# Optimization experiments

Measured on AMD Instinct MI355X. Metric: run time of the kernel, lower is better.

Reference implementation:

```python
import jax, jax.numpy as jnp
import numpy as np

B, S, H, D = 1, 2048, 16, 128
CAUSAL = True


def setup_inputs() -> dict:
    key = jax.random.key(0)
    kq, kk, kv = jax.random.split(key, 3)
    query = jax.random.normal(kq, (B, S, H, D), dtype=jnp.float32)
    k_ = jax.random.normal(kk, (B, S, H, D), dtype=jnp.float32)
    v_ = jax.random.normal(kv, (B, S, H, D), dtype=jnp.float32)
    return {"query": query, "key": k_, "value": v_}


def reference(query, key, value):
    # Single-device equivalent of LongContextAttention:
    # Ulysses all-to-all and ring pass are identity on one rank; the math is
    # standard scaled-dot-product attention with flash-attn's default scale
    # softmax_scale = 1/sqrt(head_dim) and causal masking.
    d = query.shape[-1]
    scale = 1.0 / jnp.sqrt(jnp.asarray(d, dtype=query.dtype))
    # [B,S,H,D] x [B,T,H,D] -> [B,H,S,T]
    scores = jnp.einsum("bshd,bthd->bhst", query, key) * scale
    if CAUSAL:
        s, t = scores.shape[-2], scores.shape[-1]
        mask = jnp.tril(jnp.ones((s, t), dtype=bool))
        scores = jnp.where(mask, scores, jnp.finfo(scores.dtype).min)
    probs = jax.nn.softmax(scores, axis=-1)
    out = jnp.einsum("bhst,bthd->bshd", probs, value)
    return out
```

## Files before the change

kernel.cpp:

```cpp
#include <hip/hip_runtime.h>
#include <hip/hip_bf16.h>
#include <math.h>

#define SS 2048
#define HH 16
#define DD 128
#define HD (HH*DD)
#define QB 128
#define KVB 64
#define CHUNK 7
#define NJ 46

typedef __attribute__((ext_vector_type(8))) short bf16x8;
typedef __attribute__((ext_vector_type(16))) float f32x16;

__device__ __forceinline__ ushort f2bf(float f) {
  __hip_bfloat16 h = __float2bfloat16(f);
  return __builtin_bit_cast(ushort, h);
}
__device__ __forceinline__ uint pk2(float a, float b) {
  return ((uint)f2bf(b) << 16) | (uint)f2bf(a);
}
__device__ __forceinline__ float bf2f(ushort u) {
  uint x = ((uint)u) << 16;
  return __builtin_bit_cast(float, x);
}
__device__ __forceinline__ void gld16(const void* g, void* l) {
  __builtin_amdgcn_global_load_lds(
      (const __attribute__((address_space(1))) void*)g,
      (__attribute__((address_space(3))) void*)l, 16, 0, 0);
}

__constant__ const int JBc[17] = {0,1,2,3,5,7,9,11,14,17,20,24,28,32,36,41,46};

__global__ __launch_bounds__(256, 4)
void prep_kv(const float* __restrict__ K, const float* __restrict__ V,
             ushort* __restrict__ Kbf, ushort* __restrict__ VTg) {
  __shared__ ushort Vlds[64][136];
  const int tid = threadIdx.x;
  const int h  = blockIdx.x & 15;
  const int tc = blockIdx.x >> 4;
  const int t0 = tc * 64;

  #pragma unroll
  for (int j = 0; j < 2; ++j) {
    int li = tid + j * 256;
    int t  = li >> 3;
    int c  = (li & 7) << 4;
    const float* src = K + ((size_t)(t0 + t) * HH + h) * DD + c;
    ushort tmp[16];
    #pragma unroll
    for (int q = 0; q < 4; ++q) {
      float4 x = *(const float4*)(src + 4 * q);
      tmp[4*q+0] = f2bf(x.x); tmp[4*q+1] = f2bf(x.y);
      tmp[4*q+2] = f2bf(x.z); tmp[4*q+3] = f2bf(x.w);
    }
    ushort* dst = Kbf + ((size_t)h * SS + t0 + t) * DD + c;
    *(uint4*)dst       = *(uint4*)&tmp[0];
    *(uint4*)(dst + 8) = *(uint4*)&tmp[8];
  }

  #pragma unroll
  for (int j = 0; j < 2; ++j) {
    int li = tid + j * 256;
    int t  = li >> 3;
    int c  = (li & 7) << 4;
    const float* src = V + ((size_t)(t0 + t) * HH + h) * DD + c;
    #pragma unroll
    for (int q = 0; q < 4; ++q) {
      float4 x = *(const float4*)(src + 4 * q);
      ushort4 w; w.x = f2bf(x.x); w.y = f2bf(x.y); w.z = f2bf(x.z); w.w = f2bf(x.w);
      *(ushort4*)&Vlds[t][c + 4 * q] = w;
    }
  }
  __syncthreads();

  #pragma unroll
  for (int j = 0; j < 2; ++j) {
    int li  = tid + j * 256;
    int d   = li >> 2;
    int t16 = (li & 3) << 4;
    ushort tmp[16];
    #pragma unroll
    for (int k = 0; k < 16; ++k) tmp[k] = Vlds[t16 + k][d];
    ushort* dst = VTg + (((size_t)h * 32 + tc) * DD + d) * 64 + t16;
    *(uint4*)dst       = *(uint4*)&tmp[0];
    *(uint4*)(dst + 8) = *(uint4*)&tmp[8];
  }
}

__global__ __launch_bounds__(256, 2)
void attn_fwd(const float* __restrict__ Q, const ushort* __restrict__ Kbf,
              const ushort* __restrict__ VTg, float* __restrict__ O,
              ushort* __restrict__ PO, float* __restrict__ PM,
              float* __restrict__ PL) {
  __shared__ alignas(16) ushort Klds[2][KVB * DD];
  __shared__ alignas(16) ushort VTlds[2][DD * KVB];

  const int tid  = threadIdx.x;
  const int lane = tid & 63;
  const int wid  = tid >> 6;
  const int q32  = lane & 31;
  const int hi   = lane >> 5;
  const int kxk  = (q32 & 15) << 4;
  const int kxv  = ((q32 & 7) << 4) ^ ((q32 & 8) << 1);

  int koff[4], voff[4];
  #pragma unroll
  for (int k2 = 0; k2 < 4; ++k2) {
    int b = wid * 4096 + k2 * 1024 + 16 * lane;
    int krow = b >> 8;
    koff[k2] = b ^ ((krow & 15) << 4);
    int d = b >> 7;
    voff[k2] = b ^ (((d & 7) << 4) ^ ((d & 8) << 1));
  }

  const int bx = blockIdx.x;
  const int h  = bx & 15;
  const int j  = bx >> 4;
  int qt = 0, c = 0;
  #pragma unroll
  for (int q2 = 15; q2 >= 0; --q2) {
    if (j >= JBc[q2]) { qt = q2; c = j - JBc[q2]; break; }
  }
  const int nt  = 2 * qt + 2;
  const int lo  = CHUNK * c;
  const int hiT = min(lo + CHUNK, nt);
  const int nc  = JBc[qt + 1] - JBc[qt];

  const float SCALE = 1.44269504088896f / sqrtf((float)DD);
  const char* KG = (const char*)Kbf + (size_t)h * SS * DD * 2;
  const char* VG = (const char*)VTg + (size_t)h * 32 * 16384;

  auto issueK = [&](int t0, int buf) {
    const char* gt = KG + (size_t)t0 * 256;
    char* lb = (char*)&Klds[buf][0] + wid * 4096;
    #pragma unroll
    for (int k2 = 0; k2 < 4; ++k2)
      gld16(gt + koff[k2], lb + k2 * 1024);
  };
  auto issueV = [&](int tc, int buf) {
    const char* gt = VG + (size_t)tc * 16384;
    char* lb = (char*)&VTlds[buf][0] + wid * 4096;
    #pragma unroll
    for (int k2 = 0; k2 < 4; ++k2)
      gld16(gt + voff[k2], lb + k2 * 1024);
  };

  const int qw = qt * QB + 32 * wid;
  const int qg = qw + q32;

  bf16x8 qf[8];
  {
    const float* qr = Q + ((size_t)qg * HH + h) * DD;
    #pragma unroll
    for (int ks = 0; ks < 8; ++ks) {
      float4 x = *(const float4*)&qr[16 * ks + 8 * hi];
      float4 y = *(const float4*)&qr[16 * ks + 8 * hi + 4];
      uint4 u;
      u.x = pk2(x.x * SCALE, x.y * SCALE);
      u.y = pk2(x.z * SCALE, x.w * SCALE);
      u.z = pk2(y.x * SCALE, y.y * SCALE);
      u.w = pk2(y.z * SCALE, y.w * SCALE);
      qf[ks] = __builtin_bit_cast(bf16x8, u);
    }
  }

  f32x16 acc[4];
  #pragma unroll
  for (int dt = 0; dt < 4; ++dt)
    #pragma unroll
    for (int e = 0; e < 16; ++e) acc[dt][e] = 0.f;
  float m = -1e30f, l = 0.f;

  issueK(lo * KVB, 0);
  issueV(lo, 0);
  int cur = 0;

  for (int itile = lo; itile < hiT; ++itile) {
    __syncthreads();
    const bool more = (itile + 1 < hiT);
    if (more) {
      issueK((itile + 1) * KVB, cur ^ 1);
      issueV(itile + 1, cur ^ 1);
    }

    const int t0 = itile * KVB;
    const char* Kc = (const char*)&Klds[cur][0];
    const char* Vc = (const char*)&VTlds[cur][0];

    f32x16 s0, s1;
    #pragma unroll
    for (int e = 0; e < 16; ++e) { s0[e] = 0.f; s1[e] = 0.f; }
    __builtin_amdgcn_s_setprio(1);
    #pragma unroll
    for (int ks = 0; ks < 8; ++ks) {
      bf16x8 a0 = *(const bf16x8*)(Kc + ((q32 * 256 + 32 * ks + 16 * hi) ^ kxk));
      s0 = __builtin_amdgcn_mfma_f32_32x32x16_bf16(a0, qf[ks], s0, 0, 0, 0);
      bf16x8 a1 = *(const bf16x8*)(Kc + (((q32 + 32) * 256 + 32 * ks + 16 * hi) ^ kxk));
      s1 = __builtin_amdgcn_mfma_f32_32x32x16_bf16(a1, qf[ks], s1, 0, 0, 0);
    }
    __builtin_amdgcn_s_setprio(0);

    if (t0 + KVB - 1 > qw) {
      #pragma unroll
      for (int e = 0; e < 16; ++e) {
        int tloc = (e & 3) + 8 * (e >> 2) + 4 * hi;
        if (t0 + tloc > qg)      s0[e] = -INFINITY;
        if (t0 + 32 + tloc > qg) s1[e] = -INFINITY;
      }
    }

    float tmx[8];
    #pragma unroll
    for (int e = 0; e < 8; ++e)
      tmx[e] = fmaxf(fmaxf(s0[e], s0[e + 8]), fmaxf(s1[e], s1[e + 8]));
    #pragma unroll
    for (int st = 4; st >= 1; st >>= 1)
      #pragma unroll
      for (int e = 0; e < st; ++e) tmx[e] = fmaxf(tmx[e], tmx[e + st]);
    float mr = fmaxf(tmx[0], __shfl_xor(tmx[0], 32));

    if (!__all(mr <= m + 8.0f)) {
      float mn = fmaxf(m, mr);
      float corr = exp2f(m - mn);
      m = mn;
      l *= corr;
      #pragma unroll
      for (int dt = 0; dt < 4; ++dt)
        #pragma unroll
        for (int e = 0; e < 16; ++e) acc[dt][e] *= corr;
    }

    float ts[8];
    #pragma unroll
    for (int e = 0; e < 8; ++e) ts[e] = 0.f;
    #pragma unroll
    for (int e = 0; e < 16; ++e) {
      float p0 = exp2f(s0[e] - m); s0[e] = p0;
      float p1 = exp2f(s1[e] - m); s1[e] = p1;
      ts[e & 7] += p0 + p1;
    }
    #pragma unroll
    for (int st = 4; st >= 1; st >>= 1)
      #pragma unroll
      for (int e = 0; e < st; ++e) ts[e] += ts[e + st];
    float ps = ts[0] + __shfl_xor(ts[0], 32);
    l += ps;

    uint4 paf[4];
    #pragma unroll
    for (int tk = 0; tk < 4; ++tk) {
      float p0,p1,p2,p3,p4,p5,p6,p7;
      if (tk == 0) { p0=s0[0];p1=s0[1];p2=s0[2];p3=s0[3];p4=s0[4];p5=s0[5];p6=s0[6];p7=s0[7]; }
      else if (tk == 1) { p0=s0[8];p1=s0[9];p2=s0[10];p3=s0[11];p4=s0[12];p5=s0[13];p6=s0[14];p7=s0[15]; }
      else if (tk == 2) { p0=s1[0];p1=s1[1];p2=s1[2];p3=s1[3];p4=s1[4];p5=s1[5];p6=s1[6];p7=s1[7]; }
      else { p0=s1[8];p1=s1[9];p2=s1[10];p3=s1[11];p4=s1[12];p5=s1[13];p6=s1[14];p7=s1[15]; }
      uint A0 = pk2(p0, p1), A1 = pk2(p2, p3);
      uint B0 = pk2(p4, p5), B1 = pk2(p6, p7);
      uint x0 = hi ? A0 : B0, x1 = hi ? A1 : B1;
      uint r0 = (uint)__shfl_xor((int)x0, 32);
      uint r1 = (uint)__shfl_xor((int)x1, 32);
      paf[tk].x = hi ? r0 : A0;
      paf[tk].y = hi ? r1 : A1;
      paf[tk].z = hi ? B0 : r0;
      paf[tk].w = hi ? B1 : r1;
    }

    __builtin_amdgcn_s_setprio(1);
    #pragma unroll
    for (int tk = 0; tk < 4; ++tk) {
      bf16x8 pb = __builtin_bit_cast(bf16x8, paf[tk]);
      #pragma unroll
      for (int dt = 0; dt < 4; ++dt) {
        bf16x8 va = *(const bf16x8*)(Vc +
                      (((dt * 32 + q32) * 128 + 32 * tk + 16 * hi) ^ kxv));
        acc[dt] = __builtin_amdgcn_mfma_f32_32x32x16_bf16(va, pb, acc[dt], 0, 0, 0);
      }
    }
    __builtin_amdgcn_s_setprio(0);

    cur ^= 1;
  }

  const int row = 32 * wid + q32;
  if (nc == 1) {
    float invl = 1.0f / l;
    float* op = O + ((size_t)(qt * QB + row) * HH + h) * DD;
    #pragma unroll
    for (int dt = 0; dt < 4; ++dt) {
      #pragma unroll
      for (int rq = 0; rq < 4; ++rq) {
        int d = 32 * dt + 8 * rq + 4 * hi;
        float4 x = make_float4(acc[dt][4 * rq + 0] * invl, acc[dt][4 * rq + 1] * invl,
                               acc[dt][4 * rq + 2] * invl, acc[dt][4 * rq + 3] * invl);
        *(float4*)&op[d] = x;
      }
    }
  } else {
    ushort* po = PO + (size_t)bx * (QB * DD);
    #pragma unroll
    for (int dt = 0; dt < 4; ++dt) {
      #pragma unroll
      for (int rq = 0; rq < 4; ++rq) {
        int d = 32 * dt + 8 * rq + 4 * hi;
        uint2 w;
        w.x = pk2(acc[dt][4 * rq + 0], acc[dt][4 * rq + 1]);
        w.y = pk2(acc[dt][4 * rq + 2], acc[dt][4 * rq + 3]);
        *(uint2*)&po[row * DD + d] = w;
      }
    }
    if (hi == 0) {
      PM[(size_t)bx * QB + row] = m;
      PL[(size_t)bx * QB + row] = l;
    }
  }
}

__global__ __launch_bounds__(256, 2)
void attn_merge(const ushort* __restrict__ PO, const float* __restrict__ PM,
                const float* __restrict__ PL, float* __restrict__ O) {
  const int bx  = blockIdx.x;
  const int h   = bx & 15;
  const int qt  = 3 + (bx >> 4);
  const int tid = threadIdx.x;
  const int r   = tid >> 1;
  const int dh  = (tid & 1) * 64;

  const int base = JBc[qt];
  const int nc   = JBc[qt + 1] - JBc[qt];

  float M = -1e30f;
  for (int cc = 0; cc < nc; ++cc) {
    int slot = (base + cc) * 16 + h;
    M = fmaxf(M, PM[(size_t)slot * QB + r]);
  }
  float L = 0.f;
  float o[64];
  #pragma unroll
  for (int k2 = 0; k2 < 64; ++k2) o[k2] = 0.f;
  for (int cc = 0; cc < nc; ++cc) {
    int slot = (base + cc) * 16 + h;
    float w = exp2f(PM[(size_t)slot * QB + r] - M);
    L += PL[(size_t)slot * QB + r] * w;
    const ushort* src = PO + (size_t)slot * (QB * DD) + r * DD + dh;
    #pragma unroll
    for (int k4 = 0; k4 < 16; ++k4) {
      ushort4 u = *(const ushort4*)&src[4 * k4];
      o[4*k4+0] += bf2f(u.x) * w;
      o[4*k4+1] += bf2f(u.y) * w;
      o[4*k4+2] += bf2f(u.z) * w;
      o[4*k4+3] += bf2f(u.w) * w;
    }
  }
  float inv = 1.0f / L;
  float* op = O + ((size_t)(qt * QB + r) * HH + h) * DD + dh;
  #pragma unroll
  for (int k4 = 0; k4 < 16; ++k4) {
    float4 x = make_float4(o[4*k4]*inv, o[4*k4+1]*inv, o[4*k4+2]*inv, o[4*k4+3]*inv);
    *(float4*)&op[4 * k4] = x;
  }
}

extern "C" void kernel_launch(void* const* d_in, const int* in_sizes, int n_in,
                              void* d_out, int out_size, void* d_ws, size_t ws_size,
                              hipStream_t stream) {
  const float* Q = (const float*)d_in[0];
  const float* K = (const float*)d_in[1];
  const float* V = (const float*)d_in[2];
  float* O = (float*)d_out;

  const size_t kv_elems = (size_t)HH * SS * DD;
  ushort* Kbf = (ushort*)d_ws;
  ushort* VTg = Kbf + kv_elems;
  ushort* PO  = VTg + kv_elems;
  float*  PM  = (float*)(PO + (size_t)(NJ * 16) * QB * DD);
  float*  PL  = PM + (size_t)(NJ * 16) * QB;

  prep_kv<<<dim3(HH * (SS / 64)), 256, 0, stream>>>(K, V, Kbf, VTg);
  attn_fwd<<<dim3(NJ * 16), 256, 0, stream>>>(Q, Kbf, VTg, O, PO, PM, PL);
  attn_merge<<<dim3(13 * 16), 256, 0, stream>>>(PO, PM, PL, O);
}
```

Measured before the change: 78.66 us.

## Convert K to bf16 inside attention kernel and rebalance split-KV work chunks

Removes the K conversion from the prep kernel. The attention kernel now loads fp32 K into registers, packs it to bf16 and stores it into swizzled LDS mid-iteration, so the load overlaps with compute. The split-KV partition changes from fixed 7-tile chunks to an even split per query tile (38 work items), and blocks are launched heaviest-first by reversing the index. This trades a K prep pass and its global round trip for more register pressure and doubled fp32 K reads per block.

Measured after the change: 77.46 us. Within noise of the previous version (-1.5%).

```diff
diff --git a/kernel.cpp b/kernel.cpp
--- a/kernel.cpp
+++ b/kernel.cpp
@@ -8,8 +8,7 @@
 #define HD (HH*DD)
 #define QB 128
 #define KVB 64
-#define CHUNK 7
-#define NJ 46
+#define NJ 38
 
 typedef __attribute__((ext_vector_type(8))) short bf16x8;
 typedef __attribute__((ext_vector_type(16))) float f32x16;
@@ -31,11 +30,10 @@
       (__attribute__((address_space(3))) void*)l, 16, 0, 0);
 }
 
-__constant__ const int JBc[17] = {0,1,2,3,5,7,9,11,14,17,20,24,28,32,36,41,46};
+__constant__ const int JB2c[17] = {0,1,2,3,4,6,8,10,12,14,17,20,23,26,30,34,38};
 
 __global__ __launch_bounds__(256, 4)
-void prep_kv(const float* __restrict__ K, const float* __restrict__ V,
-             ushort* __restrict__ Kbf, ushort* __restrict__ VTg) {
+void prep_v(const float* __restrict__ V, ushort* __restrict__ VTg) {
   __shared__ ushort Vlds[64][136];
   const int tid = threadIdx.x;
   const int h  = blockIdx.x & 15;
@@ -47,24 +45,6 @@
     int li = tid + j * 256;
     int t  = li >> 3;
     int c  = (li & 7) << 4;
-    const float* src = K + ((size_t)(t0 + t) * HH + h) * DD + c;
-    ushort tmp[16];
-    #pragma unroll
-    for (int q = 0; q < 4; ++q) {
-      float4 x = *(const float4*)(src + 4 * q);
-      tmp[4*q+0] = f2bf(x.x); tmp[4*q+1] = f2bf(x.y);
-      tmp[4*q+2] = f2bf(x.z); tmp[4*q+3] = f2bf(x.w);
-    }
-    ushort* dst = Kbf + ((size_t)h * SS + t0 + t) * DD + c;
-    *(uint4*)dst       = *(uint4*)&tmp[0];
-    *(uint4*)(dst + 8) = *(uint4*)&tmp[8];
-  }
-
-  #pragma unroll
-  for (int j = 0; j < 2; ++j) {
-    int li = tid + j * 256;
-    int t  = li >> 3;
-    int c  = (li & 7) << 4;
     const float* src = V + ((size_t)(t0 + t) * HH + h) * DD + c;
     #pragma unroll
     for (int q = 0; q < 4; ++q) {
@@ -90,7 +70,7 @@
 }
 
 __global__ __launch_bounds__(256, 2)
-void attn_fwd(const float* __restrict__ Q, const ushort* __restrict__ Kbf,
+void attn_fwd(const float* __restrict__ Q, const float* __restrict__ K,
               const ushort* __restrict__ VTg, float* __restrict__ O,
               ushort* __restrict__ PO, float* __restrict__ PM,
               float* __restrict__ PL) {
@@ -105,39 +85,50 @@
   const int kxk  = (q32 & 15) << 4;
   const int kxv  = ((q32 & 7) << 4) ^ ((q32 & 8) << 1);
 
-  int koff[4], voff[4];
+  int voff[4];
   #pragma unroll
   for (int k2 = 0; k2 < 4; ++k2) {
     int b = wid * 4096 + k2 * 1024 + 16 * lane;
-    int krow = b >> 8;
-    koff[k2] = b ^ ((krow & 15) << 4);
     int d = b >> 7;
     voff[k2] = b ^ (((d & 7) << 4) ^ ((d & 8) << 1));
   }
 
   const int bx = blockIdx.x;
   const int h  = bx & 15;
-  const int j  = bx >> 4;
+  const int jrev = (NJ - 1) - (bx >> 4);
   int qt = 0, c = 0;
   #pragma unroll
   for (int q2 = 15; q2 >= 0; --q2) {
-    if (j >= JBc[q2]) { qt = q2; c = j - JBc[q2]; break; }
+    if (jrev >= JB2c[q2]) { qt = q2; c = jrev - JB2c[q2]; break; }
   }
   const int nt  = 2 * qt + 2;
-  const int lo  = CHUNK * c;
-  const int hiT = min(lo + CHUNK, nt);
-  const int nc  = JBc[qt + 1] - JBc[qt];
+  const int nc  = JB2c[qt + 1] - JB2c[qt];
+  const int lo  = (c * nt) / nc;
+  const int hiT = ((c + 1) * nt) / nc;
 
   const float SCALE = 1.44269504088896f / sqrtf((float)DD);
-  const char* KG = (const char*)Kbf + (size_t)h * SS * DD * 2;
-  const char* VG = (const char*)VTg + (size_t)h * 32 * 16384;
-
-  auto issueK = [&](int t0, int buf) {
-    const char* gt = KG + (size_t)t0 * 256;
-    char* lb = (char*)&Klds[buf][0] + wid * 4096;
-    #pragma unroll
-    for (int k2 = 0; k2 < 4; ++k2)
-      gld16(gt + koff[k2], lb + k2 * 1024);
+  const float* Kb = K + (size_t)h * DD;
+  const char*  VG = (const char*)VTg + (size_t)h * 32 * 16384;
+
+  uint4 kreg[4];
+  auto loadK = [&](int t0) {
+    #pragma unroll
+    for (int it = 0; it < 4; ++it) {
+      int e = tid + it * 256;
+      int row = e >> 4, col = (e & 15) * 8;
+      const float* src = &Kb[(size_t)(t0 + row) * HD + col];
+      float4 a = *(const float4*)src;
+      float4 b = *(const float4*)(src + 4);
+      kreg[it].x = pk2(a.x, a.y); kreg[it].y = pk2(a.z, a.w);
+      kreg[it].z = pk2(b.x, b.y); kreg[it].w = pk2(b.z, b.w);
+    }
+  };
+  auto stageK = [&](int buf) {
+    #pragma unroll
+    for (int it = 0; it < 4; ++it) {
+      int e = tid + it * 256;
+      *(uint4*)((char*)&Klds[buf][0] + ((e * 16) ^ (e & 0xF0))) = kreg[it];
+    }
   };
   auto issueV = [&](int tc, int buf) {
     const char* gt = VG + (size_t)tc * 16384;
@@ -173,16 +164,17 @@
     for (int e = 0; e < 16; ++e) acc[dt][e] = 0.f;
   float m = -1e30f, l = 0.f;
 
-  issueK(lo * KVB, 0);
+  loadK(lo * KVB);
   issueV(lo, 0);
+  stageK(0);
   int cur = 0;
 
   for (int itile = lo; itile < hiT; ++itile) {
     __syncthreads();
     const bool more = (itile + 1 < hiT);
     if (more) {
-      issueK((itile + 1) * KVB, cur ^ 1);
       issueV(itile + 1, cur ^ 1);
+      loadK((itile + 1) * KVB);
     }
 
     const int t0 = itile * KVB;
@@ -267,6 +259,8 @@
       paf[tk].w = hi ? B1 : r1;
     }
 
+    if (more) stageK(cur ^ 1);
+
     __builtin_amdgcn_s_setprio(1);
     #pragma unroll
     for (int tk = 0; tk < 4; ++tk) {
@@ -322,17 +316,16 @@
                 const float* __restrict__ PL, float* __restrict__ O) {
   const int bx  = blockIdx.x;
   const int h   = bx & 15;
-  const int qt  = 3 + (bx >> 4);
+  const int qt  = 4 + (bx >> 4);
   const int tid = threadIdx.x;
   const int r   = tid >> 1;
   const int dh  = (tid & 1) * 64;
 
-  const int base = JBc[qt];
-  const int nc   = JBc[qt + 1] - JBc[qt];
+  const int nc = JB2c[qt + 1] - JB2c[qt];
 
   float M = -1e30f;
   for (int cc = 0; cc < nc; ++cc) {
-    int slot = (base + cc) * 16 + h;
+    int slot = h + 16 * ((NJ - 1) - (JB2c[qt] + cc));
     M = fmaxf(M, PM[(size_t)slot * QB + r]);
   }
   float L = 0.f;
@@ -340,7 +333,7 @@
   #pragma unroll
   for (int k2 = 0; k2 < 64; ++k2) o[k2] = 0.f;
   for (int cc = 0; cc < nc; ++cc) {
-    int slot = (base + cc) * 16 + h;
+    int slot = h + 16 * ((NJ - 1) - (JB2c[qt] + cc));
     float w = exp2f(PM[(size_t)slot * QB + r] - M);
     L += PL[(size_t)slot * QB + r] * w;
     const ushort* src = PO + (size_t)slot * (QB * DD) + r * DD + dh;
@@ -371,13 +364,12 @@
   float* O = (float*)d_out;
 
   const size_t kv_elems = (size_t)HH * SS * DD;
-  ushort* Kbf = (ushort*)d_ws;
-  ushort* VTg = Kbf + kv_elems;
+  ushort* VTg = (ushort*)d_ws;
   ushort* PO  = VTg + kv_elems;
   float*  PM  = (float*)(PO + (size_t)(NJ * 16) * QB * DD);
   float*  PL  = PM + (size_t)(NJ * 16) * QB;
 
-  prep_kv<<<dim3(HH * (SS / 64)), 256, 0, stream>>>(K, V, Kbf, VTg);
-  attn_fwd<<<dim3(NJ * 16), 256, 0, stream>>>(Q, Kbf, VTg, O, PO, PM, PL);
-  attn_merge<<<dim3(13 * 16), 256, 0, stream>>>(PO, PM, PL, O);
-}
+  prep_v<<<dim3(HH * (SS / 64)), 256, 0, stream>>>(V, VTg);
+  attn_fwd<<<dim3(NJ * 16), 256, 0, stream>>>(Q, K, VTg, O, PO, PM, PL);
+  attn_merge<<<dim3(12 * 16), 256, 0, stream>>>(PO, PM, PL, O);
+}
```
